# Kernel optimization log

Measured on AMD Instinct MI355X. Metric: run time of the kernel, lower is better.

## Reference

```python
import jax, jax.numpy as jnp
import numpy as np

N = 50000        # number of nodes (A is [N, N] sparse adjacency)
NNZ = 1600000    # number of edges (avg degree 32)
UNITS = 64       # output feature dim


def setup_inputs() -> dict:
    key = jax.random.key(0)
    k1, k2, k3, k4 = jax.random.split(key, 4)
    rows = jax.random.randint(k1, (NNZ,), 0, N, dtype=jnp.int32)
    cols = jax.random.randint(k2, (NNZ,), 0, N, dtype=jnp.int32)
    values = jax.random.uniform(k3, (NNZ,), dtype=jnp.float32)
    # glorot-like scale for kernel of shape (N, UNITS)
    kernel = jax.random.normal(k4, (N, UNITS), dtype=jnp.float32) * np.float32(1.0 / np.sqrt(N))
    bias = jnp.zeros((UNITS,), dtype=jnp.float32)
    return {"rows": rows, "cols": cols, "values": values, "kernel": kernel, "bias": bias}


def reference(rows, cols, values, kernel, bias):
    # Faithful math of: relu(dense(A) @ kernel + bias), computed as SpMM
    # (zeros of the densified A contribute nothing, so results are identical).
    gathered = values[:, None] * kernel[cols]           # [nnz, units]
    out = jax.ops.segment_sum(gathered, rows, num_segments=N)  # [N, units]
    return jax.nn.relu(out + bias)
```

## Files before the change

kernel.cpp:

```cpp
#include <hip/hip_runtime.h>

#define UNITS 64
#define NNODES 50000
#define NBUCK 512
#define CAP 3584
#define BIN_TPB 512
#define BIN_EPT 8
#define PREP_BLOCKS 782
#define SPMM_TPB 1024

typedef unsigned long long u64;
typedef unsigned int u32;
typedef unsigned short u16;


__device__ __forceinline__ int rowbase_of(u32 b) {
    return (int)((b * 50000u + 511u) >> 9);
}

__device__ __forceinline__ u16 f2bf(u32 b) {
    return (u16)((b + 0x7FFFu + ((b >> 16) & 1u)) >> 16);
}

__global__ __launch_bounds__(BIN_TPB) void gc_bin_prep(const int* __restrict__ rows,
                                                       const int* __restrict__ cols,
                                                       const float* __restrict__ values,
                                                       const float* __restrict__ kf,
                                                       u16* __restrict__ kb,
                                                       int* __restrict__ gcursor,
                                                       u64* __restrict__ edges,
                                                       int nnz, int binBlocks) {
    int t = threadIdx.x;
    if ((int)blockIdx.x >= binBlocks) {
        int base = ((blockIdx.x - binBlocks) * BIN_TPB + t) * 8;
        if (base + 8 <= NNODES * UNITS) {
            float4 fa = ((const float4*)(kf + base))[0];
            float4 fb = ((const float4*)(kf + base))[1];
            ushort4 oa, ob;
            oa.x = f2bf(__float_as_uint(fa.x)); oa.y = f2bf(__float_as_uint(fa.y));
            oa.z = f2bf(__float_as_uint(fa.z)); oa.w = f2bf(__float_as_uint(fa.w));
            ob.x = f2bf(__float_as_uint(fb.x)); ob.y = f2bf(__float_as_uint(fb.y));
            ob.z = f2bf(__float_as_uint(fb.z)); ob.w = f2bf(__float_as_uint(fb.w));
            ((ushort4*)(kb + base))[0] = oa;
            ((ushort4*)(kb + base))[1] = ob;
        }
        return;
    }

    __shared__ u64 stage[BIN_TPB * BIN_EPT];
    __shared__ int hist[NBUCK];
    __shared__ int lstart[NBUCK];
    __shared__ int delta[NBUCK];
    __shared__ int wsum[8];
    hist[t] = 0;
    __syncthreads();

    int blockStart = blockIdx.x * (BIN_TPB * BIN_EPT);
    int cnt = min(BIN_TPB * BIN_EPT, nnz - blockStart);
    int base_idx = blockStart + t * BIN_EPT;

    int rr[BIN_EPT];
    int cc[BIN_EPT];
    float vv[BIN_EPT];
    if (base_idx + BIN_EPT <= nnz) {
        int4 ra = ((const int4*)(rows + base_idx))[0];
        int4 rb = ((const int4*)(rows + base_idx))[1];
        int4 ca = ((const int4*)(cols + base_idx))[0];
        int4 cb = ((const int4*)(cols + base_idx))[1];
        float4 va = ((const float4*)(values + base_idx))[0];
        float4 vb = ((const float4*)(values + base_idx))[1];
        rr[0]=ra.x; rr[1]=ra.y; rr[2]=ra.z; rr[3]=ra.w;
        rr[4]=rb.x; rr[5]=rb.y; rr[6]=rb.z; rr[7]=rb.w;
        cc[0]=ca.x; cc[1]=ca.y; cc[2]=ca.z; cc[3]=ca.w;
        cc[4]=cb.x; cc[5]=cb.y; cc[6]=cb.z; cc[7]=cb.w;
        vv[0]=va.x; vv[1]=va.y; vv[2]=va.z; vv[3]=va.w;
        vv[4]=vb.x; vv[5]=vb.y; vv[6]=vb.z; vv[7]=vb.w;
    } else {
#pragma unroll
        for (int k = 0; k < BIN_EPT; ++k) {
            int idx = base_idx + k;
            rr[k] = (idx < nnz) ? rows[idx] : -1;
            cc[k] = (idx < nnz) ? cols[idx] : 0;
            vv[k] = (idx < nnz) ? values[idx] : 0.0f;
        }
    }

    u64 rec[BIN_EPT];
    int bk[BIN_EPT];
    int rk[BIN_EPT];
#pragma unroll
    for (int k = 0; k < BIN_EPT; ++k) {
        if (rr[k] >= 0) {
            int r = rr[k];
            u32 v = __float_as_uint(vv[k]);
            int b = (int)(((u32)r * 512u) / 50000u);
            int lrow = r - rowbase_of((u32)b);
            rec[k] = ((u64)v << 32) | ((u64)(u32)b << 23) | ((u64)(u32)lrow << 16) | (u64)(u32)cc[k];
            bk[k] = b;
            rk[k] = atomicAdd(&hist[b], 1);
        } else {
            bk[k] = -1;
        }
    }
    __syncthreads();

    {
        int wid = t >> 6, ln = t & 63;
        int val = hist[t];
        for (int off = 1; off < 64; off <<= 1) {
            int x = __shfl_up(val, off, 64);
            if (ln >= off) val += x;
        }
        if (ln == 63) wsum[wid] = val;
        __syncthreads();
        if (t == 0) {
            int s = 0;
            for (int i = 0; i < 8; ++i) { int x = wsum[i]; wsum[i] = s; s += x; }
        }
        __syncthreads();
        int incl = val + wsum[wid];
        int excl = incl - hist[t];
        int h = hist[t];
        int gbase = (h > 0) ? (t * CAP + atomicAdd(&gcursor[t], h)) : 0;
        delta[t] = gbase - excl;
        lstart[t] = excl;
    }
    __syncthreads();

#pragma unroll
    for (int k = 0; k < BIN_EPT; ++k) {
        if (bk[k] >= 0) stage[lstart[bk[k]] + rk[k]] = rec[k];
    }
    __syncthreads();

    for (int i = t; i < cnt; i += BIN_TPB) {
        u64 r = stage[i];
        int b = (int)((r >> 23) & 0x1FF);
        int gpos = delta[b] + i;
        if (gpos < (b + 1) * CAP) edges[gpos] = r;
    }
}

__global__ __launch_bounds__(SPMM_TPB) void gc_spmm(const u64* __restrict__ edges,
                                                    const int* __restrict__ gcursor,
                                                    const u16* __restrict__ kb,
                                                    const float* __restrict__ bias,
                                                    float* __restrict__ out) {
    __shared__ u64 stage[CAP];
    __shared__ int rhist[128];
    __shared__ int rstart[129];
    __shared__ int wsum2[2];
    int b = blockIdx.x;
    int t = threadIdx.x;
    int rowlo = rowbase_of((u32)b);
    int nrows = rowbase_of((u32)b + 1u) - rowlo;
    int count = min(gcursor[b], CAP);
    const u64* eb = edges + (size_t)b * CAP;

    if (t < 128) rhist[t] = 0;
    __syncthreads();

    u64 rec[4];
    int rk[4], lr[4];
#pragma unroll
    for (int k = 0; k < 4; ++k) {
        int i = k * SPMM_TPB + t;
        if (i < count) {
            u64 r = eb[i];
            rec[k] = r;
            int l = (int)((r >> 16) & 0x7F);
            lr[k] = l;
            rk[k] = atomicAdd(&rhist[l], 1);
        } else {
            lr[k] = -1;
        }
    }
    __syncthreads();

    {
        int wid = t >> 6, ln = t & 63;
        int val = (t < 128) ? rhist[t] : 0;
        if (wid < 2) {
            for (int off = 1; off < 64; off <<= 1) {
                int x = __shfl_up(val, off, 64);
                if (ln >= off) val += x;
            }
            if (ln == 63) wsum2[wid] = val;
        }
        __syncthreads();
        if (t == 0) { int a = wsum2[0]; wsum2[0] = 0; wsum2[1] = a; }
        __syncthreads();
        if (wid < 2) rstart[t] = val + wsum2[wid] - rhist[t];
        if (t == 0) rstart[128] = count;
    }
    __syncthreads();

#pragma unroll
    for (int k = 0; k < 4; ++k) {
        if (lr[k] >= 0) stage[rstart[lr[k]] + rk[k]] = rec[k];
    }
    __syncthreads();

    int lane = t & 63;
    int ep = lane >> 4;
    int uq = lane & 15;
    int w = t >> 6;
    float4 bl = ((const float4*)bias)[uq];

    for (int row = w; row < nrows; row += 16) {
        int j0 = rstart[row];
        int e  = rstart[row + 1];
        float ax0=0.f, ay0=0.f, az0=0.f, aw0=0.f;
        float ax1=0.f, ay1=0.f, az1=0.f, aw1=0.f;
        float ax2=0.f, ay2=0.f, az2=0.f, aw2=0.f;
        float ax3=0.f, ay3=0.f, az3=0.f, aw3=0.f;
        int j = j0;
        for (; j + 16 <= e; j += 16) {
            u64 r0 = stage[j + 0  + ep];
            u64 r1 = stage[j + 4  + ep];
            u64 r2 = stage[j + 8  + ep];
            u64 r3 = stage[j + 12 + ep];
            u64 q0 = *(const u64*)(kb + ((u32)r0 & 0xFFFFu) * UNITS + 4 * uq);
            u64 q1 = *(const u64*)(kb + ((u32)r1 & 0xFFFFu) * UNITS + 4 * uq);
            u64 q2 = *(const u64*)(kb + ((u32)r2 & 0xFFFFu) * UNITS + 4 * uq);
            u64 q3 = *(const u64*)(kb + ((u32)r3 & 0xFFFFu) * UNITS + 4 * uq);
            float v0 = __uint_as_float((u32)(r0 >> 32));
            float v1 = __uint_as_float((u32)(r1 >> 32));
            float v2 = __uint_as_float((u32)(r2 >> 32));
            float v3 = __uint_as_float((u32)(r3 >> 32));
            u32 lo, hi;
            lo = (u32)q0; hi = (u32)(q0 >> 32);
            ax0 = fmaf(v0, __uint_as_float(lo << 16), ax0);
            ay0 = fmaf(v0, __uint_as_float(lo & 0xFFFF0000u), ay0);
            az0 = fmaf(v0, __uint_as_float(hi << 16), az0);
            aw0 = fmaf(v0, __uint_as_float(hi & 0xFFFF0000u), aw0);
            lo = (u32)q1; hi = (u32)(q1 >> 32);
            ax1 = fmaf(v1, __uint_as_float(lo << 16), ax1);
            ay1 = fmaf(v1, __uint_as_float(lo & 0xFFFF0000u), ay1);
            az1 = fmaf(v1, __uint_as_float(hi << 16), az1);
            aw1 = fmaf(v1, __uint_as_float(hi & 0xFFFF0000u), aw1);
            lo = (u32)q2; hi = (u32)(q2 >> 32);
            ax2 = fmaf(v2, __uint_as_float(lo << 16), ax2);
            ay2 = fmaf(v2, __uint_as_float(lo & 0xFFFF0000u), ay2);
            az2 = fmaf(v2, __uint_as_float(hi << 16), az2);
            aw2 = fmaf(v2, __uint_as_float(hi & 0xFFFF0000u), aw2);
            lo = (u32)q3; hi = (u32)(q3 >> 32);
            ax3 = fmaf(v3, __uint_as_float(lo << 16), ax3);
            ay3 = fmaf(v3, __uint_as_float(lo & 0xFFFF0000u), ay3);
            az3 = fmaf(v3, __uint_as_float(hi << 16), az3);
            aw3 = fmaf(v3, __uint_as_float(hi & 0xFFFF0000u), aw3);
        }
        for (; j < e; j += 4) {
            int ji = j + ep;
            float v = 0.f;
            u64 q = 0;
            if (ji < e) {
                u64 r = stage[ji];
                q = *(const u64*)(kb + ((u32)r & 0xFFFFu) * UNITS + 4 * uq);
                v = __uint_as_float((u32)(r >> 32));
            }
            u32 lo = (u32)q, hi = (u32)(q >> 32);
            ax0 = fmaf(v, __uint_as_float(lo << 16), ax0);
            ay0 = fmaf(v, __uint_as_float(lo & 0xFFFF0000u), ay0);
            az0 = fmaf(v, __uint_as_float(hi << 16), az0);
            aw0 = fmaf(v, __uint_as_float(hi & 0xFFFF0000u), aw0);
        }
        float ax = (ax0 + ax1) + (ax2 + ax3);
        float ay = (ay0 + ay1) + (ay2 + ay3);
        float az = (az0 + az1) + (az2 + az3);
        float aw = (aw0 + aw1) + (aw2 + aw3);
        ax += __shfl_xor(ax, 16, 64); ax += __shfl_xor(ax, 32, 64);
        ay += __shfl_xor(ay, 16, 64); ay += __shfl_xor(ay, 32, 64);
        az += __shfl_xor(az, 16, 64); az += __shfl_xor(az, 32, 64);
        aw += __shfl_xor(aw, 16, 64); aw += __shfl_xor(aw, 32, 64);
        if (ep == 0) {
            float4 o;
            o.x = fmaxf(ax + bl.x, 0.0f);
            o.y = fmaxf(ay + bl.y, 0.0f);
            o.z = fmaxf(az + bl.z, 0.0f);
            o.w = fmaxf(aw + bl.w, 0.0f);
            ((float4*)out)[(size_t)(rowlo + row) * 16 + uq] = o;
        }
    }
}

extern "C" void kernel_launch(void* const* d_in, const int* in_sizes, int n_in,
                              void* d_out, int out_size, void* d_ws, size_t ws_size,
                              hipStream_t stream) {
    const int*   rows   = (const int*)d_in[0];
    const int*   cols   = (const int*)d_in[1];
    const float* values = (const float*)d_in[2];
    const float* kern   = (const float*)d_in[3];
    const float* bias   = (const float*)d_in[4];
    float* out = (float*)d_out;

    const int nnz = in_sizes[0];

    char* ws = (char*)d_ws;
    u16* kb      = (u16*)(ws + 0);
    int* gcursor = (int*)(ws + 6400000);
    u64* edges   = (u64*)(ws + 6402048);

    hipMemsetAsync(gcursor, 0, NBUCK * sizeof(int), stream);

    int binBlocks = (nnz + BIN_TPB * BIN_EPT - 1) / (BIN_TPB * BIN_EPT);
    gc_bin_prep<<<binBlocks + PREP_BLOCKS, BIN_TPB, 0, stream>>>(
        rows, cols, values, kern, kb, gcursor, edges, nnz, binBlocks);

    gc_spmm<<<NBUCK, SPMM_TPB, 0, stream>>>(edges, gcursor, kb, bias, out);
}
```

Measured before the change: 118.1 us.

## Assign one 16-lane group per row in SpMM to drop cross-lane reduction

The SpMM work mapping changes from one wavefront per row, where four edge partitions are combined with shuffles, to one 16-thread group per row, so each wavefront handles four rows. Each group walks its row's edges serially in steps of four with a single accumulator set, which removes the shuffle reduction and the idle lanes on short rows. Launch bounds now request a minimum of 8 blocks per multiprocessor, which caps register use. The cost is a longer dependent FMA chain per thread, and rows of unequal length now diverge within a wavefront.

Result: no change. 118.9 us (+0.7%).

```diff
diff --git a/kernel.cpp b/kernel.cpp
--- a/kernel.cpp
+++ b/kernel.cpp
@@ -141,11 +141,11 @@
     }
 }
 
-__global__ __launch_bounds__(SPMM_TPB) void gc_spmm(const u64* __restrict__ edges,
-                                                    const int* __restrict__ gcursor,
-                                                    const u16* __restrict__ kb,
-                                                    const float* __restrict__ bias,
-                                                    float* __restrict__ out) {
+__global__ __launch_bounds__(SPMM_TPB, 8) void gc_spmm(const u64* __restrict__ edges,
+                                                       const int* __restrict__ gcursor,
+                                                       const u16* __restrict__ kb,
+                                                       const float* __restrict__ bias,
+                                                       float* __restrict__ out) {
     __shared__ u64 stage[CAP];
     __shared__ int rhist[128];
     __shared__ int rstart[129];
@@ -201,86 +201,67 @@
     }
     __syncthreads();
 
-    int lane = t & 63;
-    int ep = lane >> 4;
-    int uq = lane & 15;
-    int w = t >> 6;
+    int uq = t & 15;
+    int g  = t >> 4;
     float4 bl = ((const float4*)bias)[uq];
-
-    for (int row = w; row < nrows; row += 16) {
+    const u16* kbq = kb + 4 * uq;
+
+    for (int row = g; row < nrows; row += 64) {
         int j0 = rstart[row];
         int e  = rstart[row + 1];
-        float ax0=0.f, ay0=0.f, az0=0.f, aw0=0.f;
-        float ax1=0.f, ay1=0.f, az1=0.f, aw1=0.f;
-        float ax2=0.f, ay2=0.f, az2=0.f, aw2=0.f;
-        float ax3=0.f, ay3=0.f, az3=0.f, aw3=0.f;
+        float ax = 0.f, ay = 0.f, az = 0.f, aw = 0.f;
         int j = j0;
-        for (; j + 16 <= e; j += 16) {
-            u64 r0 = stage[j + 0  + ep];
-            u64 r1 = stage[j + 4  + ep];
-            u64 r2 = stage[j + 8  + ep];
-            u64 r3 = stage[j + 12 + ep];
-            u64 q0 = *(const u64*)(kb + ((u32)r0 & 0xFFFFu) * UNITS + 4 * uq);
-            u64 q1 = *(const u64*)(kb + ((u32)r1 & 0xFFFFu) * UNITS + 4 * uq);
-            u64 q2 = *(const u64*)(kb + ((u32)r2 & 0xFFFFu) * UNITS + 4 * uq);
-            u64 q3 = *(const u64*)(kb + ((u32)r3 & 0xFFFFu) * UNITS + 4 * uq);
+        for (; j + 4 <= e; j += 4) {
+            u64 r0 = stage[j + 0];
+            u64 r1 = stage[j + 1];
+            u64 r2 = stage[j + 2];
+            u64 r3 = stage[j + 3];
+            u64 q0 = *(const u64*)(kbq + ((u32)r0 & 0xFFFFu) * UNITS);
+            u64 q1 = *(const u64*)(kbq + ((u32)r1 & 0xFFFFu) * UNITS);
+            u64 q2 = *(const u64*)(kbq + ((u32)r2 & 0xFFFFu) * UNITS);
+            u64 q3 = *(const u64*)(kbq + ((u32)r3 & 0xFFFFu) * UNITS);
             float v0 = __uint_as_float((u32)(r0 >> 32));
             float v1 = __uint_as_float((u32)(r1 >> 32));
             float v2 = __uint_as_float((u32)(r2 >> 32));
             float v3 = __uint_as_float((u32)(r3 >> 32));
             u32 lo, hi;
             lo = (u32)q0; hi = (u32)(q0 >> 32);
-            ax0 = fmaf(v0, __uint_as_float(lo << 16), ax0);
-            ay0 = fmaf(v0, __uint_as_float(lo & 0xFFFF0000u), ay0);
-            az0 = fmaf(v0, __uint_as_float(hi << 16), az0);
-            aw0 = fmaf(v0, __uint_as_float(hi & 0xFFFF0000u), aw0);
+            ax = fmaf(v0, __uint_as_float(lo << 16), ax);
+            ay = fmaf(v0, __uint_as_float(lo & 0xFFFF0000u), ay);
+            az = fmaf(v0, __uint_as_float(hi << 16), az);
+            aw = fmaf(v0, __uint_as_float(hi & 0xFFFF0000u), aw);
             lo = (u32)q1; hi = (u32)(q1 >> 32);
-            ax1 = fmaf(v1, __uint_as_float(lo << 16), ax1);
-            ay1 = fmaf(v1, __uint_as_float(lo & 0xFFFF0000u), ay1);
-            az1 = fmaf(v1, __uint_as_float(hi << 16), az1);
-            aw1 = fmaf(v1, __uint_as_float(hi & 0xFFFF0000u), aw1);
+            ax = fmaf(v1, __uint_as_float(lo << 16), ax);
+            ay = fmaf(v1, __uint_as_float(lo & 0xFFFF0000u), ay);
+            az = fmaf(v1, __uint_as_float(hi << 16), az);
+            aw = fmaf(v1, __uint_as_float(hi & 0xFFFF0000u), aw);
             lo = (u32)q2; hi = (u32)(q2 >> 32);
-            ax2 = fmaf(v2, __uint_as_float(lo << 16), ax2);
-            ay2 = fmaf(v2, __uint_as_float(lo & 0xFFFF0000u), ay2);
-            az2 = fmaf(v2, __uint_as_float(hi << 16), az2);
-            aw2 = fmaf(v2, __uint_as_float(hi & 0xFFFF0000u), aw2);
+            ax = fmaf(v2, __uint_as_float(lo << 16), ax);
+            ay = fmaf(v2, __uint_as_float(lo & 0xFFFF0000u), ay);
+            az = fmaf(v2, __uint_as_float(hi << 16), az);
+            aw = fmaf(v2, __uint_as_float(hi & 0xFFFF0000u), aw);
             lo = (u32)q3; hi = (u32)(q3 >> 32);
-            ax3 = fmaf(v3, __uint_as_float(lo << 16), ax3);
-            ay3 = fmaf(v3, __uint_as_float(lo & 0xFFFF0000u), ay3);
-            az3 = fmaf(v3, __uint_as_float(hi << 16), az3);
-            aw3 = fmaf(v3, __uint_as_float(hi & 0xFFFF0000u), aw3);
-        }
-        for (; j < e; j += 4) {
-            int ji = j + ep;
-            float v = 0.f;
-            u64 q = 0;
-            if (ji < e) {
-                u64 r = stage[ji];
-                q = *(const u64*)(kb + ((u32)r & 0xFFFFu) * UNITS + 4 * uq);
-                v = __uint_as_float((u32)(r >> 32));
-            }
+            ax = fmaf(v3, __uint_as_float(lo << 16), ax);
+            ay = fmaf(v3, __uint_as_float(lo & 0xFFFF0000u), ay);
+            az = fmaf(v3, __uint_as_float(hi << 16), az);
+            aw = fmaf(v3, __uint_as_float(hi & 0xFFFF0000u), aw);
+        }
+        for (; j < e; ++j) {
+            u64 r = stage[j];
+            u64 q = *(const u64*)(kbq + ((u32)r & 0xFFFFu) * UNITS);
+            float v = __uint_as_float((u32)(r >> 32));
             u32 lo = (u32)q, hi = (u32)(q >> 32);
-            ax0 = fmaf(v, __uint_as_float(lo << 16), ax0);
-            ay0 = fmaf(v, __uint_as_float(lo & 0xFFFF0000u), ay0);
-            az0 = fmaf(v, __uint_as_float(hi << 16), az0);
-            aw0 = fmaf(v, __uint_as_float(hi & 0xFFFF0000u), aw0);
-        }
-        float ax = (ax0 + ax1) + (ax2 + ax3);
-        float ay = (ay0 + ay1) + (ay2 + ay3);
-        float az = (az0 + az1) + (az2 + az3);
-        float aw = (aw0 + aw1) + (aw2 + aw3);
-        ax += __shfl_xor(ax, 16, 64); ax += __shfl_xor(ax, 32, 64);
-        ay += __shfl_xor(ay, 16, 64); ay += __shfl_xor(ay, 32, 64);
-        az += __shfl_xor(az, 16, 64); az += __shfl_xor(az, 32, 64);
-        aw += __shfl_xor(aw, 16, 64); aw += __shfl_xor(aw, 32, 64);
-        if (ep == 0) {
-            float4 o;
-            o.x = fmaxf(ax + bl.x, 0.0f);
-            o.y = fmaxf(ay + bl.y, 0.0f);
-            o.z = fmaxf(az + bl.z, 0.0f);
-            o.w = fmaxf(aw + bl.w, 0.0f);
-            ((float4*)out)[(size_t)(rowlo + row) * 16 + uq] = o;
-        }
+            ax = fmaf(v, __uint_as_float(lo << 16), ax);
+            ay = fmaf(v, __uint_as_float(lo & 0xFFFF0000u), ay);
+            az = fmaf(v, __uint_as_float(hi << 16), az);
+            aw = fmaf(v, __uint_as_float(hi & 0xFFFF0000u), aw);
+        }
+        float4 o;
+        o.x = fmaxf(ax + bl.x, 0.0f);
+        o.y = fmaxf(ay + bl.y, 0.0f);
+        o.z = fmaxf(az + bl.z, 0.0f);
+        o.w = fmaxf(aw + bl.w, 0.0f);
+        ((float4*)out)[(size_t)(rowlo + row) * 16 + uq] = o;
     }
 }
 
```
